# Optimization experiments

Measured on AMD Instinct MI355X. Metric: run time of the kernel, lower is better.

## Reference

```python
import jax, jax.numpy as jnp
import numpy as np

N_NODES = 100000
D_FEAT = 128
N_EDGES = 600000


def setup_inputs() -> dict:
    key = jax.random.key(0)
    k1, k2, k3 = jax.random.split(key, 3)
    z1 = jax.random.normal(k1, (N_NODES, D_FEAT), dtype=jnp.float32)
    z2 = jax.random.normal(k2, (N_NODES, D_FEAT), dtype=jnp.float32)
    edge_index = jax.random.randint(k3, (2, N_EDGES), 0, N_NODES, dtype=jnp.int64)
    return {"z1": z1, "z2": z2, "edge_index": edge_index}


def reference(z1, z2, edge_index):
    # Gather endpoint embeddings per edge, inner product, sigmoid.
    src = z1[edge_index[0]]  # [E, d]
    dst = z2[edge_index[1]]  # [E, d]
    logits = jnp.sum(src * dst, axis=1)  # [E]
    return jax.nn.sigmoid(logits)
```

## Files before the change

### kernel.cpp

```cpp
#include <hip/hip_runtime.h>
#include <hip/hip_bf16.h>
#include <hip/hip_fp16.h>
#include <math.h>


#define D_FEAT 128

__global__ __launch_bounds__(256) void convert_kernel(
    const float* __restrict__ z1, const float* __restrict__ z2,
    __half* __restrict__ z1h, __half* __restrict__ z2h, int n8) {
  const int i = blockIdx.x * blockDim.x + threadIdx.x;
  const int which = (i < n8) ? 0 : 1;
  const int j = which ? (i - n8) : i;
  if (i >= 2 * n8) return;
  const float* src = which ? z2 : z1;
  __half* dst = which ? z2h : z1h;

  const float4* p = (const float4*)src + 2 * (size_t)j;
  const float4 a = p[0];
  const float4 b = p[1];
  union { __half2 h[4]; float4 f; } u;
  u.h[0] = __floats2half2_rn(a.x, a.y);
  u.h[1] = __floats2half2_rn(a.z, a.w);
  u.h[2] = __floats2half2_rn(b.x, b.y);
  u.h[3] = __floats2half2_rn(b.z, b.w);
  ((float4*)dst)[j] = u.f;
}

#define LANES_H 16
#define EPG 4

__global__ __launch_bounds__(256) void ipd_h_kernel(
    const __half* __restrict__ z1h, const __half* __restrict__ z2h,
    const int* __restrict__ edge_index, float* __restrict__ out, int n_edges) {
  const int tid = blockIdx.x * blockDim.x + threadIdx.x;
  const int lane = tid & (LANES_H - 1);
  const int group = tid / LANES_H;
  const int ebase = group * EPG;
  if (ebase >= n_edges) return;

  const int4 s4 = *(const int4*)(edge_index + ebase);
  const int4 d4 = *(const int4*)(edge_index + n_edges + ebase);
  const int s[EPG] = {s4.x, s4.y, s4.z, s4.w};
  const int d[EPG] = {d4.x, d4.y, d4.z, d4.w};

  float4 va[EPG], vb[EPG];
#pragma unroll
  for (int i = 0; i < EPG; ++i) {
    va[i] = ((const float4*)(z1h + (size_t)s[i] * D_FEAT))[lane];
    vb[i] = ((const float4*)(z2h + (size_t)d[i] * D_FEAT))[lane];
  }

  float sum[EPG];
#pragma unroll
  for (int i = 0; i < EPG; ++i) {
    const __half2* ha = (const __half2*)&va[i];
    const __half2* hb = (const __half2*)&vb[i];
    float acc = 0.f;
#pragma unroll
    for (int k = 0; k < 4; ++k) {
      const float2 fa = __half22float2(ha[k]);
      const float2 fb = __half22float2(hb[k]);
      acc += fa.x * fb.x + fa.y * fb.y;
    }
    sum[i] = acc;
  }

#pragma unroll
  for (int off = LANES_H / 2; off > 0; off >>= 1) {
#pragma unroll
    for (int i = 0; i < EPG; ++i) sum[i] += __shfl_xor(sum[i], off, LANES_H);
  }

  if (lane == 0) {
    float4 o;
    o.x = 1.0f / (1.0f + __expf(-sum[0]));
    o.y = 1.0f / (1.0f + __expf(-sum[1]));
    o.z = 1.0f / (1.0f + __expf(-sum[2]));
    o.w = 1.0f / (1.0f + __expf(-sum[3]));
    *(float4*)(out + ebase) = o;
  }
}

#define LANES_F 32

__global__ __launch_bounds__(256) void ipd_f_kernel(
    const float* __restrict__ z1, const float* __restrict__ z2,
    const int* __restrict__ edge_index, float* __restrict__ out, int n_edges) {
  const int tid = blockIdx.x * blockDim.x + threadIdx.x;
  const int lane = tid & (LANES_F - 1);
  const int group = tid / LANES_F;
  const int ebase = group * EPG;
  if (ebase >= n_edges) return;

  const int4 s4 = *(const int4*)(edge_index + ebase);
  const int4 d4 = *(const int4*)(edge_index + n_edges + ebase);
  const int s[EPG] = {s4.x, s4.y, s4.z, s4.w};
  const int d[EPG] = {d4.x, d4.y, d4.z, d4.w};

  float4 va[EPG], vb[EPG];
#pragma unroll
  for (int i = 0; i < EPG; ++i) {
    va[i] = ((const float4*)(z1 + (size_t)s[i] * D_FEAT))[lane];
    vb[i] = ((const float4*)(z2 + (size_t)d[i] * D_FEAT))[lane];
  }

  float sum[EPG];
#pragma unroll
  for (int i = 0; i < EPG; ++i)
    sum[i] = va[i].x * vb[i].x + va[i].y * vb[i].y +
             va[i].z * vb[i].z + va[i].w * vb[i].w;

#pragma unroll
  for (int off = LANES_F / 2; off > 0; off >>= 1) {
#pragma unroll
    for (int i = 0; i < EPG; ++i) sum[i] += __shfl_xor(sum[i], off, LANES_F);
  }

  if (lane == 0) {
    float4 o;
    o.x = 1.0f / (1.0f + __expf(-sum[0]));
    o.y = 1.0f / (1.0f + __expf(-sum[1]));
    o.z = 1.0f / (1.0f + __expf(-sum[2]));
    o.w = 1.0f / (1.0f + __expf(-sum[3]));
    *(float4*)(out + ebase) = o;
  }
}

extern "C" void kernel_launch(void* const* d_in, const int* in_sizes, int n_in,
                              void* d_out, int out_size, void* d_ws, size_t ws_size,
                              hipStream_t stream) {
  const float* z1 = (const float*)d_in[0];
  const float* z2 = (const float*)d_in[1];
  const int* edge_index = (const int*)d_in[2];
  float* out = (float*)d_out;

  const int n_edges = in_sizes[2] / 2;
  const int n_feat_elems = in_sizes[0];

  const size_t half_bytes = (size_t)n_feat_elems * sizeof(__half);

  const int block = 256;

  if (ws_size >= 2 * half_bytes && (n_feat_elems % 8) == 0) {
    __half* z1h = (__half*)d_ws;
    __half* z2h = (__half*)((char*)d_ws + half_bytes);

    const int n8 = n_feat_elems / 8;
    const int cgrid = (2 * n8 + block - 1) / block;
    convert_kernel<<<cgrid, block, 0, stream>>>(z1, z2, z1h, z2h, n8);

    const int groups = (n_edges + EPG - 1) / EPG;
    const long long total = (long long)groups * LANES_H;
    const int grid = (int)((total + block - 1) / block);
    ipd_h_kernel<<<grid, block, 0, stream>>>(z1h, z2h, edge_index, out, n_edges);
  } else {
    const int groups = (n_edges + EPG - 1) / EPG;
    const long long total = (long long)groups * LANES_F;
    const int grid = (int)((total + block - 1) / block);
    ipd_f_kernel<<<grid, block, 0, stream>>>(z1, z2, edge_index, out, n_edges);
  }
}
```

Before: 168.1 us.

## Use grid-stride loop with index prefetch and fdot2 in half-precision gather kernel

Result: no change. 170.1 us (+1.2%).

```diff
diff --git a/kernel.cpp b/kernel.cpp
--- a/kernel.cpp
+++ b/kernel.cpp
@@ -6,13 +6,15 @@
 
 #define D_FEAT 128
 
+typedef _Float16 half2v __attribute__((ext_vector_type(2)));
+
 __global__ __launch_bounds__(256) void convert_kernel(
     const float* __restrict__ z1, const float* __restrict__ z2,
     __half* __restrict__ z1h, __half* __restrict__ z2h, int n8) {
   const int i = blockIdx.x * blockDim.x + threadIdx.x;
+  if (i >= 2 * n8) return;
   const int which = (i < n8) ? 0 : 1;
   const int j = which ? (i - n8) : i;
-  if (i >= 2 * n8) return;
   const float* src = which ? z2 : z1;
   __half* dst = which ? z2h : z1h;
 
@@ -30,55 +32,118 @@
 #define LANES_H 16
 #define EPG 4
 
+__device__ __forceinline__ float dot8_h(float4 a, float4 b) {
+  const half2v* ha = (const half2v*)&a;
+  const half2v* hb = (const half2v*)&b;
+  float acc = 0.f;
+#pragma unroll
+  for (int k = 0; k < 4; ++k) {
+#if defined(__has_builtin) && __has_builtin(__builtin_amdgcn_fdot2)
+    acc = __builtin_amdgcn_fdot2(ha[k], hb[k], acc, false);
+#else
+    const float2 fa = __half22float2(((const __half2*)&a)[k]);
+    const float2 fb = __half22float2(((const __half2*)&b)[k]);
+    acc += fa.x * fb.x + fa.y * fb.y;
+#endif
+  }
+  return acc;
+}
+
+__device__ __forceinline__ float sigmoidf_(float x) {
+  return 1.0f / (1.0f + __expf(-x));
+}
+
 __global__ __launch_bounds__(256) void ipd_h_kernel(
     const __half* __restrict__ z1h, const __half* __restrict__ z2h,
-    const int* __restrict__ edge_index, float* __restrict__ out, int n_edges) {
-  const int tid = blockIdx.x * blockDim.x + threadIdx.x;
-  const int lane = tid & (LANES_H - 1);
-  const int group = tid / LANES_H;
-  const int ebase = group * EPG;
-  if (ebase >= n_edges) return;
-
-  const int4 s4 = *(const int4*)(edge_index + ebase);
-  const int4 d4 = *(const int4*)(edge_index + n_edges + ebase);
-  const int s[EPG] = {s4.x, s4.y, s4.z, s4.w};
-  const int d[EPG] = {d4.x, d4.y, d4.z, d4.w};
-
-  float4 va[EPG], vb[EPG];
-#pragma unroll
-  for (int i = 0; i < EPG; ++i) {
-    va[i] = ((const float4*)(z1h + (size_t)s[i] * D_FEAT))[lane];
-    vb[i] = ((const float4*)(z2h + (size_t)d[i] * D_FEAT))[lane];
-  }
-
-  float sum[EPG];
-#pragma unroll
-  for (int i = 0; i < EPG; ++i) {
-    const __half2* ha = (const __half2*)&va[i];
-    const __half2* hb = (const __half2*)&vb[i];
-    float acc = 0.f;
-#pragma unroll
-    for (int k = 0; k < 4; ++k) {
-      const float2 fa = __half22float2(ha[k]);
-      const float2 fb = __half22float2(hb[k]);
-      acc += fa.x * fb.x + fa.y * fb.y;
-    }
-    sum[i] = acc;
-  }
-
-#pragma unroll
-  for (int off = LANES_H / 2; off > 0; off >>= 1) {
-#pragma unroll
-    for (int i = 0; i < EPG; ++i) sum[i] += __shfl_xor(sum[i], off, LANES_H);
-  }
-
-  if (lane == 0) {
-    float4 o;
-    o.x = 1.0f / (1.0f + __expf(-sum[0]));
-    o.y = 1.0f / (1.0f + __expf(-sum[1]));
-    o.z = 1.0f / (1.0f + __expf(-sum[2]));
-    o.w = 1.0f / (1.0f + __expf(-sum[3]));
-    *(float4*)(out + ebase) = o;
+    const int* __restrict__ edge_index, float* __restrict__ out,
+    int n_edges, int ngroups) {
+  const int lane = threadIdx.x & (LANES_H - 1);
+  const int lane_b = lane << 4;
+  int g = (blockIdx.x * blockDim.x + threadIdx.x) >> 4;
+  const int gstride = (gridDim.x * blockDim.x) >> 4;
+  if (g >= ngroups) return;
+
+  const int* __restrict__ srcp = edge_index;
+  const int* __restrict__ dstp = edge_index + n_edges;
+  const char* __restrict__ z1b = (const char*)z1h;
+  const char* __restrict__ z2b = (const char*)z2h;
+
+  int4 s4, d4;
+  {
+    const int rem = n_edges - g * EPG;
+    if (rem >= EPG) {
+      s4 = *(const int4*)(srcp + g * EPG);
+      d4 = *(const int4*)(dstp + g * EPG);
+    } else {
+      const int b = g * EPG;
+      s4.x = srcp[b]; d4.x = dstp[b];
+      s4.y = rem > 1 ? srcp[b + 1] : 0; d4.y = rem > 1 ? dstp[b + 1] : 0;
+      s4.z = rem > 2 ? srcp[b + 2] : 0; d4.z = rem > 2 ? dstp[b + 2] : 0;
+      s4.w = 0; d4.w = 0;
+    }
+  }
+
+  while (true) {
+    const int gn = g + gstride;
+    const bool more = gn < ngroups;
+
+    int4 s4n, d4n;
+    if (more) {
+      const int remn = n_edges - gn * EPG;
+      if (remn >= EPG) {
+        s4n = *(const int4*)(srcp + gn * EPG);
+        d4n = *(const int4*)(dstp + gn * EPG);
+      } else {
+        const int b = gn * EPG;
+        s4n.x = srcp[b]; d4n.x = dstp[b];
+        s4n.y = remn > 1 ? srcp[b + 1] : 0; d4n.y = remn > 1 ? dstp[b + 1] : 0;
+        s4n.z = remn > 2 ? srcp[b + 2] : 0; d4n.z = remn > 2 ? dstp[b + 2] : 0;
+        s4n.w = 0; d4n.w = 0;
+      }
+    }
+
+    const unsigned so[EPG] = {(unsigned)s4.x << 8, (unsigned)s4.y << 8,
+                              (unsigned)s4.z << 8, (unsigned)s4.w << 8};
+    const unsigned dofs[EPG] = {(unsigned)d4.x << 8, (unsigned)d4.y << 8,
+                                (unsigned)d4.z << 8, (unsigned)d4.w << 8};
+    float4 va[EPG], vb[EPG];
+#pragma unroll
+    for (int i = 0; i < EPG; ++i) {
+      va[i] = *(const float4*)(z1b + so[i] + lane_b);
+      vb[i] = *(const float4*)(z2b + dofs[i] + lane_b);
+    }
+
+    float sum[EPG];
+#pragma unroll
+    for (int i = 0; i < EPG; ++i) sum[i] = dot8_h(va[i], vb[i]);
+
+#pragma unroll
+    for (int off = LANES_H / 2; off > 0; off >>= 1) {
+#pragma unroll
+      for (int i = 0; i < EPG; ++i) sum[i] += __shfl_xor(sum[i], off, LANES_H);
+    }
+
+    if (lane == 0) {
+      const int ebase = g * EPG;
+      const int rem = n_edges - ebase;
+      if (rem >= EPG) {
+        float4 o;
+        o.x = sigmoidf_(sum[0]);
+        o.y = sigmoidf_(sum[1]);
+        o.z = sigmoidf_(sum[2]);
+        o.w = sigmoidf_(sum[3]);
+        *(float4*)(out + ebase) = o;
+      } else {
+        out[ebase] = sigmoidf_(sum[0]);
+        if (rem > 1) out[ebase + 1] = sigmoidf_(sum[1]);
+        if (rem > 2) out[ebase + 2] = sigmoidf_(sum[2]);
+      }
+    }
+
+    if (!more) break;
+    g = gn;
+    s4 = s4n;
+    d4 = d4n;
   }
 }
 
@@ -119,10 +184,10 @@
 
   if (lane == 0) {
     float4 o;
-    o.x = 1.0f / (1.0f + __expf(-sum[0]));
-    o.y = 1.0f / (1.0f + __expf(-sum[1]));
-    o.z = 1.0f / (1.0f + __expf(-sum[2]));
-    o.w = 1.0f / (1.0f + __expf(-sum[3]));
+    o.x = sigmoidf_(sum[0]);
+    o.y = sigmoidf_(sum[1]);
+    o.z = sigmoidf_(sum[2]);
+    o.w = sigmoidf_(sum[3]);
     *(float4*)(out + ebase) = o;
   }
 }
@@ -139,7 +204,6 @@
   const int n_feat_elems = in_sizes[0];
 
   const size_t half_bytes = (size_t)n_feat_elems * sizeof(__half);
-
   const int block = 256;
 
   if (ws_size >= 2 * half_bytes && (n_feat_elems % 8) == 0) {
@@ -150,10 +214,11 @@
     const int cgrid = (2 * n8 + block - 1) / block;
     convert_kernel<<<cgrid, block, 0, stream>>>(z1, z2, z1h, z2h, n8);
 
-    const int groups = (n_edges + EPG - 1) / EPG;
-    const long long total = (long long)groups * LANES_H;
-    const int grid = (int)((total + block - 1) / block);
-    ipd_h_kernel<<<grid, block, 0, stream>>>(z1h, z2h, edge_index, out, n_edges);
+    const int ngroups = (n_edges + EPG - 1) / EPG;
+    const long long want = ((long long)ngroups * LANES_H + block - 1) / block;
+    const int grid = (int)(want < 2048 ? want : 2048);
+    ipd_h_kernel<<<grid, block, 0, stream>>>(z1h, z2h, edge_index, out,
+                                             n_edges, ngroups);
   } else {
     const int groups = (n_edges + EPG - 1) / EPG;
     const long long total = (long long)groups * LANES_F;
```
